# Kernel optimization log

Measured on AMD Instinct MI355X. Metric: run time of the kernel, lower is better.

The kernel has to match this reference:

```python
import jax, jax.numpy as jnp
import numpy as np

# Architecture constants (from init_kwargs / mamba_ssm Mamba2 defaults)
D_MODEL = 256
D_STATE = 64
D_CONV = 4
EXPAND = 2
HEADDIM = 64
D_INNER = EXPAND * D_MODEL          # 512
NHEADS = D_INNER // HEADDIM         # 8
CONV_DIM = D_INNER + 2 * D_STATE    # 640 (ngroups=1)
D_IN_PROJ = 2 * D_INNER + 2 * D_STATE + NHEADS  # 1160
NUM_LAYERS = 4
EPS = 1e-5


def _mamba2_block(h, ipw, cw, cb, dtb, alog, dpar, rmsw, opw):
    # h: (b, l, d_model)
    b, l, _ = h.shape
    zxbcdt = h @ ipw                                  # (b, l, D_IN_PROJ)
    z = zxbcdt[..., :D_INNER]
    xBC = zxbcdt[..., D_INNER:D_INNER + CONV_DIM]
    dt = zxbcdt[..., -NHEADS:]

    # causal depthwise conv1d over the sequence, then SiLU
    xBC = jnp.swapaxes(xBC, 1, 2)                     # (b, CONV_DIM, l)
    xBC = jax.lax.conv_general_dilated(
        xBC, cw[:, None, :], (1,), [(D_CONV - 1, 0)],
        feature_group_count=CONV_DIM)
    xBC = jax.nn.silu(xBC + cb[None, :, None])
    xBC = jnp.swapaxes(xBC, 1, 2)                     # (b, l, CONV_DIM)

    xh = xBC[..., :D_INNER].reshape(b, l, NHEADS, HEADDIM)
    Bm = xBC[..., D_INNER:D_INNER + D_STATE]          # (b, l, n)
    Cm = xBC[..., D_INNER + D_STATE:]                 # (b, l, n)

    dt = jax.nn.softplus(dt + dtb)                    # (b, l, h)
    A = -jnp.exp(alog)                                # (h,)

    def step(state, ins):
        # state: (b, h, p, n)
        x_t, dt_t, B_t, C_t = ins                     # (b,h,p),(b,h),(b,n),(b,n)
        dA = jnp.exp(dt_t * A)                        # (b, h)
        state = state * dA[:, :, None, None] + jnp.einsum('bh,bhp,bn->bhpn', dt_t, x_t, B_t)
        y = jnp.einsum('bhpn,bn->bhp', state, C_t)
        return state, y

    xs = (jnp.swapaxes(xh, 0, 1), jnp.swapaxes(dt, 0, 1),
          jnp.swapaxes(Bm, 0, 1), jnp.swapaxes(Cm, 0, 1))
    init = jnp.zeros((b, NHEADS, HEADDIM, D_STATE), h.dtype)
    _, ys = jax.lax.scan(step, init, xs)              # ys: (l, b, h, p)
    y = jnp.swapaxes(ys, 0, 1) + dpar[None, None, :, None] * xh
    y = y.reshape(b, l, D_INNER)

    # gated RMSNorm (norm(y * silu(z)) * weight), then out projection
    y = y * jax.nn.silu(z)
    y = y * jax.lax.rsqrt(jnp.mean(y * y, -1, keepdims=True) + EPS) * rmsw
    return y @ opw


def setup_inputs() -> dict:
    key = jax.random.key(0)
    ks = jax.random.split(key, 12)
    B, L, F = 16, 2048, 46
    inp = {
        'x': jax.random.normal(ks[0], (B, L, F), jnp.float32),
        'inp_w': jax.random.normal(ks[1], (F, D_MODEL), jnp.float32) * 0.1,
        'inp_b': jnp.zeros((D_MODEL,), jnp.float32),
        'in_proj_w': jax.random.normal(ks[2], (NUM_LAYERS, D_MODEL, D_IN_PROJ), jnp.float32) * 0.02,
        'conv_w': jax.random.normal(ks[3], (NUM_LAYERS, CONV_DIM, D_CONV), jnp.float32) * 0.2,
        'conv_b': jnp.zeros((NUM_LAYERS, CONV_DIM), jnp.float32),
        'dt_bias': jax.random.normal(ks[4], (NUM_LAYERS, NHEADS), jnp.float32) * 0.5,
        'A_log': jnp.log(jax.random.uniform(ks[5], (NUM_LAYERS, NHEADS), jnp.float32, 1.0, 16.0)),
        'D': jnp.ones((NUM_LAYERS, NHEADS), jnp.float32),
        'rms_w': jnp.ones((NUM_LAYERS, D_INNER), jnp.float32),
        'out_proj_w': jax.random.normal(ks[6], (NUM_LAYERS, D_INNER, D_MODEL), jnp.float32) * 0.02,
        'ln_w': jnp.ones((D_MODEL,), jnp.float32),
        'ln_b': jnp.zeros((D_MODEL,), jnp.float32),
        'dir_w': jax.random.normal(ks[7], (D_MODEL, 1), jnp.float32) * 0.05,
        'dir_b': jnp.zeros((1,), jnp.float32),
        'reg_w': jax.random.normal(ks[8], (D_MODEL, 3), jnp.float32) * 0.05,
        'reg_b': jnp.zeros((3,), jnp.float32),
    }
    return inp


def reference(x, inp_w, inp_b, in_proj_w, conv_w, conv_b, dt_bias, A_log, D,
              rms_w, out_proj_w, ln_w, ln_b, dir_w, dir_b, reg_w, reg_b):
    h = x @ inp_w + inp_b
    for i in range(NUM_LAYERS):
        h = h + _mamba2_block(h, in_proj_w[i], conv_w[i], conv_b[i], dt_bias[i],
                              A_log[i], D[i], rms_w[i], out_proj_w[i])
    mu = jnp.mean(h, -1, keepdims=True)
    var = jnp.mean((h - mu) ** 2, -1, keepdims=True)
    h = (h - mu) * jax.lax.rsqrt(var + EPS) * ln_w + ln_b
    h = jnp.mean(h, axis=1)                           # mean-pool over sequence
    # dropout is identity in eval mode
    dir_logits = h @ dir_w + dir_b
    reg_out = h @ reg_w + reg_b
    return (dir_logits, reg_out)
```

## Files before the change

kernel.cpp:

```cpp
#include <hip/hip_runtime.h>
#include <hip/hip_bf16.h>
#include <math.h>

typedef __hip_bfloat16 bf16;

#define B_ 16
#define L_ 2048
#define DM 256
#define DI 512
#define NH 8
#define HD 64
#define DS 64
#define CD 640
#define DIP 1160
#define XB 648
#define NP 1280
#define NL 4
#define Q_ 64
#define NCH 32
#define MROWS (B_*L_)
#define EPS_ 1e-5f
#define NIN 17
#define NSMALL 14
#define STGOFF 32
#define WIPT 28552
#define WOPT 683912
#define HMPOFF 946056
#define SLICEOFF 1011592
#define PERROW 2004

__device__ __forceinline__ float u2f(unsigned short u){ return __uint_as_float(((unsigned)u)<<16); }
__device__ __forceinline__ unsigned short f2bu(float f){ bf16 h = __float2bfloat16(f); return *(unsigned short*)&h; }
__device__ __forceinline__ float sigmoidf_(float x){ return 1.f/(1.f+__expf(-x)); }
__device__ __forceinline__ float siluf_(float x){ return x*sigmoidf_(x); }
__device__ __forceinline__ float softplusf_(float x){ return (x>20.f)? x : log1pf(__expf(x)); }

typedef __attribute__((ext_vector_type(8))) short short8v;
typedef __attribute__((ext_vector_type(4))) float float4v;
typedef __attribute__((ext_vector_type(8))) unsigned short ush8;

__device__ const int kN17[NIN] = {1507328,11776,256,1187840,10240,2560,32,32,32,2048,524288,256,256,256,1,768,3};
__device__ const int sIdx[NSMALL] = {1,2,4,5,6,7,8,9,11,12,13,14,15,16};
__device__ const int sNum[NSMALL] = {11776,256,10240,2560,32,32,32,2048,256,256,256,1,768,3};
__device__ const int sOff[NSMALL] = {0,11776,12032,22272,24832,24864,24896,24928,26976,27232,27488,27744,27748,28516};

struct PtrTab { const void* p[NIN]; };

__global__ __launch_bounds__(64) void k_sentinel(float* out, float v){
    int t = threadIdx.x;
    out[t] = (t==0) ? v : 0.f;
}

__global__ __launch_bounds__(256) void k_detect(PtrTab t, int* flags){
    int i = blockIdx.x;
    int n = kN17[i];
    int S = n < 4096 ? n : 4096;
    const unsigned short* u = (const unsigned short*)t.p[i];
    __shared__ int big, ze, zo, so;
    if (threadIdx.x == 0){ big=0; ze=0; zo=0; so=0; }
    __syncthreads();
    int lbig=0, lze=0, lzo=0, lso=0;
    for (int j=threadIdx.x; j<S; j+=256){
        unsigned short v = u[j];
        int e = (v>>7)&0xFF;
        if (e >= 131) lbig = 1;
        int isz = ((v & 0x7FFF) == 0) ? 1 : 0;
        if (j & 1){ lso++; lzo += isz; } else { lze += isz; }
    }
    if (lbig) atomicOr(&big, 1);
    atomicAdd(&ze, lze); atomicAdd(&zo, lzo); atomicAdd(&so, lso);
    __syncthreads();
    if (threadIdx.x == 0){
        int Se = S - so;
        flags[i] = (big || (so > 0 && 4*ze >= 3*Se && 4*zo <= so)) ? 1 : 0;
    }
}

__global__ __launch_bounds__(256) void k_stage(PtrTab t, const int* __restrict__ flags,
                                               float* __restrict__ stg){
    int a = blockIdx.y;
    int idx = sIdx[a];
    int n = sNum[a];
    float* dst = stg + sOff[a];
    const void* p = t.p[idx];
    if (flags[idx]){
        const float* s = (const float*)p;
        for (int j=blockIdx.x*256+threadIdx.x; j<n; j += gridDim.x*256) dst[j] = s[j];
    } else {
        const unsigned short* s = (const unsigned short*)p;
        for (int j=blockIdx.x*256+threadIdx.x; j<n; j += gridDim.x*256) dst[j] = u2f(s[j]);
    }
}

__global__ __launch_bounds__(256) void k_wip(const void* __restrict__ src,
                                             const int* __restrict__ flag,
                                             unsigned short* __restrict__ dst){
    int n = blockIdx.x, l = blockIdx.y, k = threadIdx.x;
    unsigned short b = 0;
    if (n < DIP){
        size_t si = ((size_t)l*DM + k)*DIP + n;
        if (flag[0]) b = f2bu(((const float*)src)[si]);
        else         b = ((const unsigned short*)src)[si];
    }
    dst[((size_t)l*NP + n)*DM + k] = b;
}

__global__ __launch_bounds__(256) void k_wop(const void* __restrict__ src,
                                             const int* __restrict__ flag,
                                             unsigned short* __restrict__ dst){
    int n = blockIdx.x, l = blockIdx.y;
    for (int k = threadIdx.x; k < DI; k += 256){
        size_t si = ((size_t)l*DI + k)*DM + n;
        unsigned short b;
        if (flag[0]) b = f2bu(((const float*)src)[si]);
        else         b = ((const unsigned short*)src)[si];
        dst[((size_t)l*DM + n)*DI + k] = b;
    }
}

__global__ __launch_bounds__(256) void k_zerohmp(float* __restrict__ hmp){
    hmp[(size_t)blockIdx.x*256 + threadIdx.x] = 0.f;
}

__device__ __forceinline__ float blockSum256(float v, float* red){
    #pragma unroll
    for (int off=32; off>0; off>>=1) v += __shfl_down(v, off);
    if ((threadIdx.x & 63) == 0) red[threadIdx.x >> 6] = v;
    __syncthreads();
    float s = red[0] + red[1] + red[2] + red[3];
    __syncthreads();
    return s;
}

__global__ __launch_bounds__(256) void k_inproj(const void* __restrict__ x,
                                                const int* __restrict__ flags,
                                                size_t xoff,
                                                const float* __restrict__ w,
                                                const float* __restrict__ bias,
                                                float* __restrict__ h,
                                                unsigned short* __restrict__ hbf){
    __shared__ float xs[32*46];
    int row0 = blockIdx.x*32;
    int t = threadIdx.x;
    bool f32 = flags[0] != 0;
    for (int j = t; j < 32*46; j += 256){
        size_t gi = xoff + (size_t)row0*46 + j;
        xs[j] = f32 ? ((const float*)x)[gi] : u2f(((const unsigned short*)x)[gi]);
    }
    __syncthreads();
    float bv = bias[t];
    float acc[32];
    #pragma unroll
    for (int r=0;r<32;r++) acc[r] = bv;
    for (int k=0;k<46;k++){
        float wv = w[k*DM + t];
        #pragma unroll
        for (int r=0;r<32;r++) acc[r] += xs[r*46 + k]*wv;
    }
    #pragma unroll
    for (int r=0;r<32;r++){
        size_t o = (size_t)(row0 + r)*DM + t;
        h[o] = acc[r];
        hbf[o] = f2bu(acc[r]);
    }
}

template<int MODE>
__global__ __launch_bounds__(256, 4) void k_mgemm(const unsigned short* __restrict__ A,
                                                  const unsigned short* __restrict__ Bt,
                                                  float* __restrict__ O1,
                                                  unsigned short* __restrict__ O1b,
                                                  unsigned short* __restrict__ O2b,
                                                  unsigned short* __restrict__ O3,
                                                  int K){
    __shared__ __align__(16) char ldsraw[27648];
    unsigned short* As = (unsigned short*)ldsraw;
    unsigned short* Bs = (unsigned short*)(ldsraw + 9216);
    int tid = threadIdx.x;
    int wave = tid >> 6, lane = tid & 63, quad = lane >> 4, l15 = lane & 15;
    int p = blockIdx.y * gridDim.x + blockIdx.x;
    int nwg = gridDim.x * gridDim.y;
    int cpx = nwg >> 3;
    int logical = (p & 7) * cpx + (p >> 3);
    int by = logical / gridDim.x;
    int bx = logical - by * gridDim.x;
    int mbase = by*64, nbase = bx*128;
    int wm = (wave & 1)*32, wn = (wave >> 1)*64;
    float4v zero4 = {0.f,0.f,0.f,0.f};
    float4v acc[2][4];
    #pragma unroll
    for (int mi=0;mi<2;mi++)
        #pragma unroll
        for (int ni=0;ni<4;ni++) acc[mi][ni] = zero4;

    for (int k0 = 0; k0 < K; k0 += 64){
        #pragma unroll
        for (int i=0;i<2;i++){
            int c = tid + i*256;
            int row = c >> 3, koff = (c & 7)*8;
            *(uint4*)&As[row*72 + koff] = *(const uint4*)&A[(size_t)(mbase+row)*K + k0 + koff];
        }
        #pragma unroll
        for (int i=0;i<4;i++){
            int c = tid + i*256;
            int row = c >> 3, koff = (c & 7)*8;
            *(uint4*)&Bs[row*72 + koff] = *(const uint4*)&Bt[(size_t)(nbase+row)*K + k0 + koff];
        }
        __syncthreads();
        #pragma unroll
        for (int ks=0; ks<64; ks+=32){
            short8v af[2], bfr[4];
            #pragma unroll
            for (int mi=0;mi<2;mi++) af[mi] = *(const short8v*)&As[(wm + mi*16 + l15)*72 + ks + quad*8];
            #pragma unroll
            for (int ni=0;ni<4;ni++) bfr[ni] = *(const short8v*)&Bs[(wn + ni*16 + l15)*72 + ks + quad*8];
            #pragma unroll
            for (int mi=0;mi<2;mi++)
                #pragma unroll
                for (int ni=0;ni<4;ni++)
                    acc[mi][ni] = __builtin_amdgcn_mfma_f32_16x16x32_bf16(af[mi], bfr[ni], acc[mi][ni], 0, 0, 0);
        }
        __syncthreads();
    }

    float* ep = (float*)ldsraw;
    int erow = tid >> 4;
    int ecc  = (tid & 15) * 8;
    #pragma unroll
    for (int half = 0; half < 2; ++half){
        if ((wave & 1) == half){
            #pragma unroll
            for (int mi=0;mi<2;mi++){
                #pragma unroll
                for (int ni=0;ni<4;ni++){
                    int col = wn + ni*16 + l15;
                    #pragma unroll
                    for (int reg=0;reg<4;reg++){
                        int r = mi*16 + quad*4 + reg;
                        ep[r*140 + col] = acc[mi][ni][reg];
                    }
                }
            }
        }
        __syncthreads();
        #pragma unroll
        for (int ps=0; ps<2; ps++){
            int r = ps*16 + erow;
            int growg = mbase + half*32 + r;
            int colg = nbase + ecc;
            float4 v0 = *(const float4*)&ep[r*140 + ecc + 0];
            float4 v1 = *(const float4*)&ep[r*140 + ecc + 4];
            if (MODE == 0){
                ush8 ob;
                ob[0]=f2bu(v0.x); ob[1]=f2bu(v0.y); ob[2]=f2bu(v0.z); ob[3]=f2bu(v0.w);
                ob[4]=f2bu(v1.x); ob[5]=f2bu(v1.y); ob[6]=f2bu(v1.z); ob[7]=f2bu(v1.w);
                if (colg + 8 <= DI){
                    *(ush8*)&O1b[(size_t)growg*DI + colg] = ob;
                } else if (colg >= DI && colg + 8 <= DIP){
                    *(ush8*)&O2b[(size_t)growg*XB + (colg - DI)] = ob;
                }
            } else {
                size_t ob1 = (size_t)growg*DM + colg;
                float4 h0 = *(const float4*)&O1[ob1];
                float4 h1 = *(const float4*)&O1[ob1+4];
                h0.x+=v0.x; h0.y+=v0.y; h0.z+=v0.z; h0.w+=v0.w;
                h1.x+=v1.x; h1.y+=v1.y; h1.z+=v1.z; h1.w+=v1.w;
                *(float4*)&O1[ob1] = h0;
                *(float4*)&O1[ob1+4] = h1;
                ush8 ob;
                ob[0]=f2bu(h0.x); ob[1]=f2bu(h0.y); ob[2]=f2bu(h0.z); ob[3]=f2bu(h0.w);
                ob[4]=f2bu(h1.x); ob[5]=f2bu(h1.y); ob[6]=f2bu(h1.z); ob[7]=f2bu(h1.w);
                *(ush8*)&O3[ob1] = ob;
            }
        }
        __syncthreads();
    }
}

__global__ __launch_bounds__(256) void k_conv(const unsigned short* __restrict__ xbb,
                                              const float* __restrict__ cw,
                                              const float* __restrict__ cb,
                                              const float* __restrict__ dtb,
                                              const float* __restrict__ alog,
                                              float* __restrict__ dto,
                                              float* __restrict__ cumo,
                                              unsigned short* __restrict__ cvb){
    int tid = threadIdx.x;
    if (blockIdx.x == 10){
        int r0 = blockIdx.y*64;
        int b = r0 >> 11;
        int l0 = r0 & (L_-1);
        int wave = tid >> 6, t = tid & 63;
        #pragma unroll
        for (int hh = 0; hh < 2; hh++){
            int h = wave + hh*4;
            float raw = u2f(xbb[(size_t)(r0 + t)*XB + CD + h]);
            float dtv = softplusf_(raw + dtb[h]);
            float A = -__expf(alog[h]);
            float s = dtv * A;
            #pragma unroll
            for (int off=1; off<64; off<<=1){
                float u = __shfl_up(s, off);
                if (t >= off) s += u;
            }
            int base = (b*NH + h)*L_ + l0 + t;
            dto[base] = dtv;
            cumo[base] = s;
        }
        return;
    }
    int c0 = (blockIdx.x*16 + (tid & 15))*4;
    int r0 = blockIdx.y*64 + (tid >> 4);
    float wA[4], wB[4], wC[4], wD[4];
    {
        float4 t0 = *(const float4*)&cw[(size_t)(c0+0)*4];
        float4 t1 = *(const float4*)&cw[(size_t)(c0+1)*4];
        float4 t2 = *(const float4*)&cw[(size_t)(c0+2)*4];
        float4 t3 = *(const float4*)&cw[(size_t)(c0+3)*4];
        wA[0]=t0.x; wA[1]=t0.y; wA[2]=t0.z; wA[3]=t0.w;
        wB[0]=t1.x; wB[1]=t1.y; wB[2]=t1.z; wB[3]=t1.w;
        wC[0]=t2.x; wC[1]=t2.y; wC[2]=t2.z; wC[3]=t2.w;
        wD[0]=t3.x; wD[1]=t3.y; wD[2]=t3.z; wD[3]=t3.w;
    }
    float4 bb = *(const float4*)&cb[c0];
    #pragma unroll
    for (int i=0;i<4;i++){
        int r = r0 + i*16;
        int l = r & (L_-1);
        float a0=bb.x, a1=bb.y, a2=bb.z, a3=bb.w;
        #pragma unroll
        for (int j=0;j<4;j++){
            if (l-3+j >= 0){
                ushort4 uv = *(const ushort4*)&xbb[(size_t)(r-3+j)*XB + c0];
                a0 += u2f(uv.x)*wA[j];
                a1 += u2f(uv.y)*wB[j];
                a2 += u2f(uv.z)*wC[j];
                a3 += u2f(uv.w)*wD[j];
            }
        }
        ushort4 ov;
        ov.x = f2bu(siluf_(a0));
        ov.y = f2bu(siluf_(a1));
        ov.z = f2bu(siluf_(a2));
        ov.w = f2bu(siluf_(a3));
        *(ushort4*)&cvb[(size_t)r*CD + c0] = ov;
    }
}

__device__ __forceinline__ void grp_map(int p, int &kk, int &h, int &b){
    int c = p & 7, i = p >> 3;
    h = i & 7;
    int g = (i & ~7) | c;
    kk = g & (NCH-1);
    b = g >> 5;
}

__global__ __launch_bounds__(256) void k_passS(const unsigned short* __restrict__ cvb,
                                               const float* __restrict__ dt,
                                               const float* __restrict__ cum,
                                               float* __restrict__ S){
    __shared__ unsigned short Bw[64*72];
    __shared__ unsigned short Xt[64*72];
    __shared__ float sw[64];
    int kk, h, b;
    grp_map(blockIdx.x, kk, h, b);
    int tid = threadIdx.x;
    int bh = b*NH + h;
    int l0 = kk*Q_;
    if (tid < 64){
        int base = bh*L_ + l0;
        float c = cum[base + tid];
        float c63 = cum[base + 63];
        sw[tid] = dt[base + tid]*__expf(fminf(c63 - c, 0.f));
    }
    __syncthreads();
    int srow = tid >> 4, c0 = (tid & 15)*4;
    #pragma unroll
    for (int i=0;i<4;i++){
        int s = srow + i*16;
        size_t rb = ((size_t)(b*L_ + l0 + s))*CD;
        ushort4 bv = *(const ushort4*)&cvb[rb + DI + c0];
        ushort4 xv = *(const ushort4*)&cvb[rb + h*HD + c0];
        float w = sw[s];
        Bw[(c0+0)*72 + s] = f2bu(w*u2f(bv.x));
        Bw[(c0+1)*72 + s] = f2bu(w*u2f(bv.y));
        Bw[(c0+2)*72 + s] = f2bu(w*u2f(bv.z));
        Bw[(c0+3)*72 + s] = f2bu(w*u2f(bv.w));
        Xt[(c0+0)*72 + s] = xv.x;
        Xt[(c0+1)*72 + s] = xv.y;
        Xt[(c0+2)*72 + s] = xv.z;
        Xt[(c0+3)*72 + s] = xv.w;
    }
    __syncthreads();
    int wave = tid >> 6, lane = tid & 63, quad = lane >> 4, l15 = lane & 15;
    int wn = (wave & 1)*32, wp = (wave >> 1)*32;
    float4v zero4 = {0.f,0.f,0.f,0.f};
    float4v acc[2][2];
    #pragma unroll
    for (int mi=0;mi<2;mi++)
        #pragma unroll
        for (int ni=0;ni<2;ni++) acc[mi][ni] = zero4;
    #pragma unroll
    for (int k0=0;k0<64;k0+=32){
        short8v af[2], bfr[2];
        #pragma unroll
        for (int mi=0;mi<2;mi++) af[mi] = *(const short8v*)&Bw[(wn + mi*16 + l15)*72 + k0 + quad*8];
        #pragma unroll
        for (int ni=0;ni<2;ni++) bfr[ni] = *(const short8v*)&Xt[(wp + ni*16 + l15)*72 + k0 + quad*8];
        #pragma unroll
        for (int mi=0;mi<2;mi++)
            #pragma unroll
            for (int ni=0;ni<2;ni++)
                acc[mi][ni] = __builtin_amdgcn_mfma_f32_16x16x32_bf16(af[mi], bfr[ni], acc[mi][ni], 0, 0, 0);
    }
    size_t Sbase = ((size_t)bh*NCH + kk)*4096;
    #pragma unroll
    for (int mi=0;mi<2;mi++){
        #pragma unroll
        for (int ni=0;ni<2;ni++){
            int p = wp + ni*16 + l15;
            #pragma unroll
            for (int reg=0;reg<4;reg++){
                int n = wn + mi*16 + quad*4 + reg;
                S[Sbase + n*64 + p] = acc[mi][ni][reg];
            }
        }
    }
}

__global__ __launch_bounds__(256) void k_combine(const float* __restrict__ cum,
                                                 float* __restrict__ S,
                                                 unsigned short* __restrict__ Sb){
    int h = blockIdx.x, b = blockIdx.y, z = blockIdx.z;
    int bh = b*NH + h;
    int tid = threadIdx.x;
    float4 st = make_float4(0.f,0.f,0.f,0.f);
    size_t chunk0 = ((size_t)bh*NCH)*4096;
    int qoff = z*1024 + tid*4;
    for (int k=0;k<NCH;k++){
        size_t cb = chunk0 + (size_t)k*4096;
        float dk = __expf(fminf(cum[bh*L_ + k*Q_ + 63], 0.f));
        float4 a = *(const float4*)&S[cb + qoff];
        __syncthreads();
        ushort4 pb;
        pb.x = f2bu(st.x); pb.y = f2bu(st.y); pb.z = f2bu(st.z); pb.w = f2bu(st.w);
        *(ushort4*)&Sb[2*(cb + (size_t)z*1024) + tid*4] = pb;
        st.x = a.x + dk*st.x;
        st.y = a.y + dk*st.y;
        st.z = a.z + dk*st.z;
        st.w = a.w + dk*st.w;
    }
}

__global__ __launch_bounds__(256) void k_finalize2(const unsigned short* __restrict__ cvb,
                                                   const float* __restrict__ dt,
                                                   const float* __restrict__ cum,
                                                   const float* __restrict__ Dp,
                                                   const unsigned short* __restrict__ Sb,
                                                   unsigned short* __restrict__ yB){
    __shared__ unsigned short Ct[64*72];
    __shared__ unsigned short Bs[64*72];
    __shared__ unsigned short Xt[64*72];
    __shared__ unsigned short St[64*72];
    __shared__ float sdt[64], scum[64];
    unsigned short* const Ml = &Bs[0];
    int kk, h, b;
    grp_map(blockIdx.x, kk, h, b);
    int tid = threadIdx.x;
    int bh = b*NH + h;
    int l0 = kk*Q_;
    if (tid < 64){
        int base = bh*L_ + l0;
        sdt[tid] = dt[base + tid];
        scum[tid] = cum[base + tid];
    }
    int rr = tid >> 4, c0 = (tid & 15)*4;
    size_t Sbase = ((size_t)bh*NCH + kk)*4096;
    #pragma unroll
    for (int i=0;i<4;i++){
        int r = rr + i*16;
        size_t rb = ((size_t)(b*L_ + l0 + r))*CD;
        *(ushort4*)&Ct[r*72 + c0] = *(const ushort4*)&cvb[rb + DI + DS + c0];
        *(ushort4*)&Bs[r*72 + c0] = *(const ushort4*)&cvb[rb + DI + c0];
        ushort4 xv = *(const ushort4*)&cvb[rb + h*HD + c0];
        Xt[(c0+0)*72 + r] = xv.x;
        Xt[(c0+1)*72 + r] = xv.y;
        Xt[(c0+2)*72 + r] = xv.z;
        Xt[(c0+3)*72 + r] = xv.w;
        int wfull = r*64 + c0;
        int zq = wfull >> 10;
        size_t u = 2*(Sbase + ((size_t)zq<<10)) + (wfull & 1023);
        ushort4 sv = *(const ushort4*)&Sb[u];
        St[(c0+0)*72 + r] = sv.x;
        St[(c0+1)*72 + r] = sv.y;
        St[(c0+2)*72 + r] = sv.z;
        St[(c0+3)*72 + r] = sv.w;
    }
    __syncthreads();
    int wave = tid >> 6, lane = tid & 63, quad = lane >> 4, l15 = lane & 15;
    int wt2 = (wave & 1)*32, wc = (wave >> 1)*32;
    float4v zero4 = {0.f,0.f,0.f,0.f};
    {
        float4v acc[2][2];
        #pragma unroll
        for (int mi=0;mi<2;mi++)
            #pragma unroll
            for (int ni=0;ni<2;ni++) acc[mi][ni] = zero4;
        #pragma unroll
        for (int k0=0;k0<64;k0+=32){
            short8v af[2], bfr[2];
            #pragma unroll
            for (int mi=0;mi<2;mi++) af[mi] = *(const short8v*)&Ct[(wt2 + mi*16 + l15)*72 + k0 + quad*8];
            #pragma unroll
            for (int ni=0;ni<2;ni++) bfr[ni] = *(const short8v*)&Bs[(wc + ni*16 + l15)*72 + k0 + quad*8];
            #pragma unroll
            for (int mi=0;mi<2;mi++)
                #pragma unroll
                for (int ni=0;ni<2;ni++)
                    acc[mi][ni] = __builtin_amdgcn_mfma_f32_16x16x32_bf16(af[mi], bfr[ni], acc[mi][ni], 0, 0, 0);
        }
        __syncthreads();
        #pragma unroll
        for (int mi=0;mi<2;mi++){
            #pragma unroll
            for (int ni=0;ni<2;ni++){
                int s = wc + ni*16 + l15;
                #pragma unroll
                for (int reg=0;reg<4;reg++){
                    int t = wt2 + mi*16 + quad*4 + reg;
                    float m = (s <= t) ? acc[mi][ni][reg]*sdt[s]*__expf(fminf(scum[t]-scum[s], 0.f)) : 0.f;
                    Ml[t*72 + s] = f2bu(m);
                }
            }
        }
    }
    __syncthreads();
    {
        float4v a1[2][2], a2[2][2];
        #pragma unroll
        for (int mi=0;mi<2;mi++)
            #pragma unroll
            for (int ni=0;ni<2;ni++){ a1[mi][ni] = zero4; a2[mi][ni] = zero4; }
        #pragma unroll
        for (int k0=0;k0<64;k0+=32){
            short8v mf[2], cf[2], xf[2], sf[2];
            #pragma unroll
            for (int mi=0;mi<2;mi++){
                mf[mi] = *(const short8v*)&Ml[(wt2 + mi*16 + l15)*72 + k0 + quad*8];
                cf[mi] = *(const short8v*)&Ct[(wt2 + mi*16 + l15)*72 + k0 + quad*8];
            }
            #pragma unroll
            for (int ni=0;ni<2;ni++){
                xf[ni] = *(const short8v*)&Xt[(wc + ni*16 + l15)*72 + k0 + quad*8];
                sf[ni] = *(const short8v*)&St[(wc + ni*16 + l15)*72 + k0 + quad*8];
            }
            #pragma unroll
            for (int mi=0;mi<2;mi++)
                #pragma unroll
                for (int ni=0;ni<2;ni++){
                    a1[mi][ni] = __builtin_amdgcn_mfma_f32_16x16x32_bf16(mf[mi], xf[ni], a1[mi][ni], 0, 0, 0);
                    a2[mi][ni] = __builtin_amdgcn_mfma_f32_16x16x32_bf16(cf[mi], sf[ni], a2[mi][ni], 0, 0, 0);
                }
        }
        float Dh = Dp[h];
        #pragma unroll
        for (int mi=0;mi<2;mi++){
            #pragma unroll
            for (int ni=0;ni<2;ni++){
                int p = wc + ni*16 + l15;
                #pragma unroll
                for (int reg=0;reg<4;reg++){
                    int t = wt2 + mi*16 + quad*4 + reg;
                    float e = __expf(fminf(scum[t], 0.f));
                    float xval = u2f(Xt[p*72 + t]);
                    yB[(size_t)(b*L_ + l0 + t)*DI + h*HD + p] =
                        f2bu(a1[mi][ni][reg] + e*a2[mi][ni][reg] + Dh*xval);
                }
            }
        }
    }
}

__global__ __launch_bounds__(256) void k_gaterms(const unsigned short* __restrict__ z,
                                                 const float* __restrict__ rw,
                                                 const unsigned short* __restrict__ yB,
                                                 unsigned short* __restrict__ ybf){
    __shared__ float red[4];
    int row = blockIdx.x;
    int tid = threadIdx.x;
    float g[2]; float ss = 0.f;
    #pragma unroll
    for (int r=0;r<2;r++){
        int d = tid + r*256;
        float zv = u2f(z[(size_t)row*DI + d]);
        float yv = u2f(yB[(size_t)row*DI + d]);
        float gv = yv * siluf_(zv);
        g[r] = gv;
        ss += gv*gv;
    }
    float tot = blockSum256(ss, red);
    float rinv = rsqrtf(tot*(1.f/512.f) + EPS_);
    #pragma unroll
    for (int r=0;r<2;r++){
        int d = tid + r*256;
        ybf[(size_t)row*DI + d] = f2bu(g[r]*rinv*rw[d]);
    }
}

__global__ __launch_bounds__(256) void k_lnmean(const float* __restrict__ h,
                                                const float* __restrict__ lw,
                                                const float* __restrict__ lb,
                                                float* __restrict__ hmp,
                                                int b0){
    __shared__ float red[4];
    int tid = threadIdx.x;
    int r0 = blockIdx.x*8;
    int bl = r0 >> 11;
    int g = (r0 & (L_-1)) >> 7;
    float lwv = lw[tid], lbv = lb[tid];
    float accv = 0.f;
    for (int i=0;i<8;i++){
        int row = r0 + i;
        float v = h[(size_t)row*DM + tid];
        float mu = blockSum256(v, red)*(1.f/256.f);
        float d = v - mu;
        float var = blockSum256(d*d, red)*(1.f/256.f);
        accv += d*rsqrtf(var + EPS_)*lwv + lbv;
    }
    atomicAdd(&hmp[((size_t)(b0+bl)*16 + g)*DM + tid], accv*(1.f/2048.f));
}

__global__ __launch_bounds__(256) void k_heads(const float* __restrict__ hmp,
                                               const float* __restrict__ dw,
                                               const float* __restrict__ db,
                                               const float* __restrict__ rw,
                                               const float* __restrict__ rb,
                                               float* __restrict__ out){
    __shared__ float red[4];
    int b = blockIdx.x;
    int tid = threadIdx.x;
    float hv = 0.f;
    #pragma unroll
    for (int g=0; g<16; g++) hv += hmp[((size_t)b*16 + g)*DM + tid];
    float s0 = hv*dw[tid];
    float s1 = hv*rw[tid*3+0];
    float s2 = hv*rw[tid*3+1];
    float s3 = hv*rw[tid*3+2];
    s0 = blockSum256(s0, red);
    s1 = blockSum256(s1, red);
    s2 = blockSum256(s2, red);
    s3 = blockSum256(s3, red);
    if (tid == 0){
        out[b] = s0 + db[0];
        out[16 + b*3 + 0] = s1 + rb[0];
        out[16 + b*3 + 1] = s2 + rb[1];
        out[16 + b*3 + 2] = s3 + rb[2];
    }
}

extern "C" void kernel_launch(void* const* d_in, const int* in_sizes, int n_in,
                              void* d_out, int out_size, void* d_ws, size_t ws_size,
                              hipStream_t stream){
    static const int expSizes[NIN] = {1507328,11776,256,1187840,10240,2560,32,32,32,2048,524288,256,256,256,1,768,3};
    float* out = (float*)d_out;

    if (n_in != NIN){
        k_sentinel<<<1,64,0,stream>>>(out, 9.0e6f);
        return;
    }
    for (int i=0;i<NIN;i++){
        if (in_sizes[i] != expSizes[i]){
            k_sentinel<<<1,64,0,stream>>>(out, (float)(i+1)*1.0e5f);
            return;
        }
    }
    size_t need16 = ((size_t)SLICEOFF + 2048ull*PERROW)*4ull;
    if (ws_size < need16){
        float mb = (float)(ws_size >> 20);
        k_sentinel<<<1,64,0,stream>>>(out, 2.0e7f + mb*131072.f);
        return;
    }

    float* ws = (float*)d_ws;
    int* flags = (int*)d_ws;
    float* stg = ws + STGOFF;
    unsigned short* ipwT = (unsigned short*)(ws + WIPT);
    unsigned short* opwT = (unsigned short*)(ws + WOPT);
    float* hmp = ws + HMPOFF;

    PtrTab pt;
    for (int i=0;i<NIN;i++) pt.p[i] = d_in[i];

    k_detect<<<NIN, 256, 0, stream>>>(pt, flags);
    k_stage<<<dim3(8, NSMALL), 256, 0, stream>>>(pt, flags, stg);
    k_wip<<<dim3(NP, NL), 256, 0, stream>>>(d_in[3], flags+3, ipwT);
    k_wop<<<dim3(DM, NL), 256, 0, stream>>>(d_in[10], flags+10, opwT);
    k_zerohmp<<<B_*16*DM/256, 256, 0, stream>>>(hmp);

    const float* inp_w = stg + 0;
    const float* inp_b = stg + 11776;
    const float* cw    = stg + 12032;
    const float* cb    = stg + 22272;
    const float* dtb   = stg + 24832;
    const float* alog  = stg + 24864;
    const float* Dp    = stg + 24896;
    const float* rmsw  = stg + 24928;
    const float* lnw   = stg + 26976;
    const float* lnb   = stg + 27232;
    const float* dw    = stg + 27488;
    const float* db    = stg + 27744;
    const float* rw    = stg + 27748;
    const float* rb    = stg + 28516;

    int nsl = 1;
    while (((size_t)SLICEOFF + ((size_t)MROWS/nsl)*PERROW)*4ull > ws_size) nsl <<= 1;
    const size_t R = (size_t)MROWS / nsl;
    const int SB = B_ / nsl;

    float* base = ws + SLICEOFF;
    float* hbuf = base;
    unsigned short* hbf  = (unsigned short*)(base + R*256);
    unsigned short* zb   = (unsigned short*)(base + R*384);
    unsigned short* xbb  = (unsigned short*)(base + R*640);
    unsigned short* ybB  = (unsigned short*)(base + R*640);
    unsigned short* cvb  = (unsigned short*)(base + R*964);
    unsigned short* ybf  = (unsigned short*)(base + R*964);
    float* S   = base + R*1284;
    float* dt  = base + R*1796;
    float* cum = base + R*1804;

    for (int sl=0; sl<nsl; sl++){
        k_inproj<<<(int)(R/32), 256, 0, stream>>>(d_in[0], flags, (size_t)sl*R*46, inp_w, inp_b, hbuf, hbf);
        for (int li=0; li<NL; li++){
            const float* cwl = cw + li*CD*4;
            const float* cbl = cb + li*CD;
            k_mgemm<0><<<dim3(NP/128, R/64), 256, 0, stream>>>(
                hbf, ipwT + (size_t)li*NP*DM, hbuf, zb, xbb, ybf, DM);
            k_conv<<<dim3(11, (int)(R/64)), 256, 0, stream>>>(
                xbb, cwl, cbl, dtb + li*NH, alog + li*NH, dt, cum, cvb);
            k_passS<<<NCH*NH*SB, 256, 0, stream>>>(cvb, dt, cum, S);
            k_combine<<<dim3(NH,SB,4), 256, 0, stream>>>(cum, S, (unsigned short*)S);
            k_finalize2<<<NCH*NH*SB, 256, 0, stream>>>(cvb, dt, cum, Dp + li*NH,
                (const unsigned short*)S, ybB);
            k_gaterms<<<(int)R, 256, 0, stream>>>(zb, rmsw + li*DI, ybB, ybf);
            k_mgemm<1><<<dim3(DM/128, R/64), 256, 0, stream>>>(
                ybf, opwT + (size_t)li*DM*DI, hbuf, zb, xbb, hbf, DI);
        }
        k_lnmean<<<(int)(R/8), 256, 0, stream>>>(hbuf, lnw, lnb, hmp, sl*SB);
    }
    k_heads<<<B_, 256, 0, stream>>>(hmp, dw, db, rw, rb, out);
}
```

Baseline: 985.9 us.

## Double-buffer LDS tiles with register prefetch in MFMA GEMM

Converts the GEMM main loop to a double-buffered scheme: the next K-tile is loaded from global memory into registers while MFMAs run on the current LDS tile, then written to the alternate LDS buffer, using one barrier per iteration instead of two. This is meant to hide global load latency behind compute. In exchange, LDS use doubles and launch bounds drop from 4 to 2 blocks per SM, which lowers occupancy and raises register pressure.

```diff
diff --git a/kernel.cpp b/kernel.cpp
--- a/kernel.cpp
+++ b/kernel.cpp
@@ -166,16 +166,16 @@
 }
 
 template<int MODE>
-__global__ __launch_bounds__(256, 4) void k_mgemm(const unsigned short* __restrict__ A,
+__global__ __launch_bounds__(256, 2) void k_mgemm(const unsigned short* __restrict__ A,
                                                   const unsigned short* __restrict__ Bt,
                                                   float* __restrict__ O1,
                                                   unsigned short* __restrict__ O1b,
                                                   unsigned short* __restrict__ O2b,
                                                   unsigned short* __restrict__ O3,
                                                   int K){
-    __shared__ __align__(16) char ldsraw[27648];
-    unsigned short* As = (unsigned short*)ldsraw;
-    unsigned short* Bs = (unsigned short*)(ldsraw + 9216);
+    __shared__ __align__(16) char ldsraw[55296];
+    unsigned short* AsBase = (unsigned short*)ldsraw;
+    unsigned short* BsBase = (unsigned short*)(ldsraw + 18432);
     int tid = threadIdx.x;
     int wave = tid >> 6, lane = tid & 63, quad = lane >> 4, l15 = lane & 15;
     int p = blockIdx.y * gridDim.x + blockIdx.x;
@@ -193,34 +193,60 @@
         #pragma unroll
         for (int ni=0;ni<4;ni++) acc[mi][ni] = zero4;
 
-    for (int k0 = 0; k0 < K; k0 += 64){
-        #pragma unroll
-        for (int i=0;i<2;i++){
-            int c = tid + i*256;
-            int row = c >> 3, koff = (c & 7)*8;
-            *(uint4*)&As[row*72 + koff] = *(const uint4*)&A[(size_t)(mbase+row)*K + k0 + koff];
-        }
-        #pragma unroll
-        for (int i=0;i<4;i++){
-            int c = tid + i*256;
-            int row = c >> 3, koff = (c & 7)*8;
-            *(uint4*)&Bs[row*72 + koff] = *(const uint4*)&Bt[(size_t)(nbase+row)*K + k0 + koff];
-        }
-        __syncthreads();
+    int arow[2], akf[2], brow[4], bkf[4];
+    #pragma unroll
+    for (int i=0;i<2;i++){ int c = tid + i*256; arow[i] = c >> 3; akf[i] = (c & 7)*8; }
+    #pragma unroll
+    for (int i=0;i<4;i++){ int c = tid + i*256; brow[i] = c >> 3; bkf[i] = (c & 7)*8; }
+
+    int nt = K >> 6;
+    uint4 ra[2], rb[4];
+
+    #pragma unroll
+    for (int i=0;i<2;i++) ra[i] = *(const uint4*)&A[(size_t)(mbase+arow[i])*K + akf[i]];
+    #pragma unroll
+    for (int i=0;i<4;i++) rb[i] = *(const uint4*)&Bt[(size_t)(nbase+brow[i])*K + bkf[i]];
+    #pragma unroll
+    for (int i=0;i<2;i++) *(uint4*)&AsBase[arow[i]*72 + akf[i]] = ra[i];
+    #pragma unroll
+    for (int i=0;i<4;i++) *(uint4*)&BsBase[brow[i]*72 + bkf[i]] = rb[i];
+    __syncthreads();
+
+    int cur = 0;
+    for (int t = 0; t < nt; ++t){
+        if (t+1 < nt){
+            int ko = (t+1)*64;
+            #pragma unroll
+            for (int i=0;i<2;i++) ra[i] = *(const uint4*)&A[(size_t)(mbase+arow[i])*K + ko + akf[i]];
+            #pragma unroll
+            for (int i=0;i<4;i++) rb[i] = *(const uint4*)&Bt[(size_t)(nbase+brow[i])*K + ko + bkf[i]];
+        }
+        const unsigned short* Ac = AsBase + cur*4608;
+        const unsigned short* Bc = BsBase + cur*9216;
         #pragma unroll
         for (int ks=0; ks<64; ks+=32){
             short8v af[2], bfr[4];
             #pragma unroll
-            for (int mi=0;mi<2;mi++) af[mi] = *(const short8v*)&As[(wm + mi*16 + l15)*72 + ks + quad*8];
-            #pragma unroll
-            for (int ni=0;ni<4;ni++) bfr[ni] = *(const short8v*)&Bs[(wn + ni*16 + l15)*72 + ks + quad*8];
+            for (int mi=0;mi<2;mi++) af[mi] = *(const short8v*)&Ac[(wm + mi*16 + l15)*72 + ks + quad*8];
+            #pragma unroll
+            for (int ni=0;ni<4;ni++) bfr[ni] = *(const short8v*)&Bc[(wn + ni*16 + l15)*72 + ks + quad*8];
             #pragma unroll
             for (int mi=0;mi<2;mi++)
                 #pragma unroll
                 for (int ni=0;ni<4;ni++)
                     acc[mi][ni] = __builtin_amdgcn_mfma_f32_16x16x32_bf16(af[mi], bfr[ni], acc[mi][ni], 0, 0, 0);
         }
+        if (t+1 < nt){
+            int nxt = cur ^ 1;
+            unsigned short* An = AsBase + nxt*4608;
+            unsigned short* Bn = BsBase + nxt*9216;
+            #pragma unroll
+            for (int i=0;i<2;i++) *(uint4*)&An[arow[i]*72 + akf[i]] = ra[i];
+            #pragma unroll
+            for (int i=0;i<4;i++) *(uint4*)&Bn[brow[i]*72 + bkf[i]] = rb[i];
+        }
         __syncthreads();
+        cur ^= 1;
     }
 
     float* ep = (float*)ldsraw;
```

Measured after the change: 1.312 ms. 1.33x slower.
